# Performance work log

Measured on AMD Instinct MI355X. Metric: run time of the kernel, lower is better.

Reference implementation:

```python
import jax, jax.numpy as jnp
import numpy as np

B, T, C = 4, 2048, 768   # batch, seq, n_embd
E, K = 8, 2              # n_routed_experts, moe_top_k (expert hidden dim == C per source)


def setup_inputs() -> dict:
    key = jax.random.key(0)
    ks = jax.random.split(key, 6)
    s = 0.02  # init scale to keep relu(x)^2 well-behaved
    return {
        "x": jax.random.normal(ks[0], (B, T, C), jnp.float32),
        "w_fc_sh": jax.random.normal(ks[1], (C, C), jnp.float32) * s,    # shared expert c_fc (stored [in,out])
        "w_proj_sh": jax.random.normal(ks[2], (C, C), jnp.float32) * s,  # shared expert c_proj
        "w1": jax.random.normal(ks[3], (E, C, C), jnp.float32) * s,      # routed experts c_fc, [E,in,out]
        "w2": jax.random.normal(ks[4], (E, C, C), jnp.float32) * s,      # routed experts c_proj
        "router_w": jax.random.normal(ks[5], (E, C), jnp.float32) * s,   # router weight [E, C]
        "balance_bias": jnp.zeros((E,), jnp.float32),                    # router balance_bias buffer
    }


def _mlp(x, wfc, wproj):
    # MLP: c_proj(relu(c_fc(x))**2)
    h = jnp.square(jax.nn.relu(x @ wfc))
    return h @ wproj


def reference(x, w_fc_sh, w_proj_sh, w1, w2, router_w, balance_bias):
    Bx, Tx, Cx = x.shape
    shared = _mlp(x, w_fc_sh, w_proj_sh)                    # [B,T,C]

    xf = x.reshape(-1, Cx)                                  # [N,C]
    # --- router ---
    logits = xf.astype(jnp.float32) @ router_w.T            # [N,E]
    scores = jax.nn.sigmoid(logits)
    _, idx = jax.lax.top_k(scores + balance_bias, K)        # selection uses biased scores
    tw = jnp.take_along_axis(scores, idx, axis=-1)          # gate weights from unbiased scores
    tw = tw / (tw.sum(-1, keepdims=True) + 1e-20)           # [N,K]

    # per-token per-expert combine weights (equivalent to gather/MLP/index_add loop)
    combine = (jax.nn.one_hot(idx, E, dtype=tw.dtype) * tw[..., None]).sum(1)  # [N,E]

    # dense all-expert compute, masked combine (same math as sparse dispatch)
    h = jnp.square(jax.nn.relu(jnp.einsum('nc,ech->neh', xf, w1)))  # [N,E,H]
    y = jnp.einsum('neh,ehc->nec', h, w2)                            # [N,E,C]
    routed = jnp.einsum('nec,ne->nc', y, combine)                    # [N,C]

    return shared + routed.reshape(Bx, Tx, Cx)
```

## Files before the change

kernel.cpp:

```cpp
#include <hip/hip_runtime.h>
#include <stdint.h>

#define N_TOK 8192
#define C_DIM 768
#define E_NUM 8
#define NT2 (C_DIM / 64)
#define TOTX3 104
#define GRID3 312
#define XXP3 13

typedef short short8 __attribute__((ext_vector_type(8)));
typedef __bf16 bf16x8 __attribute__((ext_vector_type(8)));
typedef float f32x4 __attribute__((ext_vector_type(4)));

static __device__ __forceinline__ unsigned short f2bf(float f) {
    unsigned u = __float_as_uint(f);
    unsigned r = u + 0x7FFFu + ((u >> 16) & 1u);
    return (unsigned short)(r >> 16);
}
static __device__ __forceinline__ float bf2f(unsigned short h) {
    return __uint_as_float(((unsigned)h) << 16);
}

__global__ void wtrans_kernel(const float* __restrict__ wfc, const float* __restrict__ wpj,
                              const float* __restrict__ w1, const float* __restrict__ w2,
                              unsigned short* __restrict__ Wt) {
    __shared__ float tile[32][33];
    const int m = blockIdx.z;
    const float* src = (m == 0) ? wfc : (m == 1) ? wpj
                     : (m < 10) ? (w1 + (size_t)(m - 2) * C_DIM * C_DIM)
                                : (w2 + (size_t)(m - 10) * C_DIM * C_DIM);
    const int i0 = blockIdx.y * 32;
    const int o0 = blockIdx.x * 32;
    #pragma unroll
    for (int rr = 0; rr < 32; rr += 8)
        tile[threadIdx.y + rr][threadIdx.x] = src[(size_t)(i0 + threadIdx.y + rr) * C_DIM + o0 + threadIdx.x];
    __syncthreads();
    unsigned short* dst = Wt + (size_t)m * C_DIM * C_DIM;
    #pragma unroll
    for (int rr = 0; rr < 32; rr += 8) {
        int o = o0 + threadIdx.y + rr;
        dst[(size_t)o * C_DIM + i0 + threadIdx.x] = f2bf(tile[threadIdx.x][threadIdx.y + rr]);
    }
}

__global__ void router_kernel(const float* __restrict__ x, const float* __restrict__ rw,
                              const float* __restrict__ bias,
                              float* __restrict__ topk_w, int* __restrict__ eids,
                              unsigned short* __restrict__ xb) {
    const int wave = threadIdx.x >> 6;
    const int lane = threadIdx.x & 63;
    const int n = blockIdx.x * 4 + wave;
    const float* xp = x + (size_t)n * C_DIM + lane * 12;
    float xv[12];
    #pragma unroll
    for (int j = 0; j < 12; j++) xv[j] = xp[j];
    unsigned short* xbp = xb + (size_t)n * C_DIM + lane * 12;
    #pragma unroll
    for (int j = 0; j < 12; j++) xbp[j] = f2bf(xv[j]);
    float acc[E_NUM];
    #pragma unroll
    for (int e = 0; e < E_NUM; e++) acc[e] = 0.f;
    #pragma unroll
    for (int e = 0; e < E_NUM; e++) {
        const float* wp = rw + (size_t)e * C_DIM + lane * 12;
        #pragma unroll
        for (int j = 0; j < 12; j++) acc[e] += xv[j] * wp[j];
    }
    #pragma unroll
    for (int e = 0; e < E_NUM; e++) {
        #pragma unroll
        for (int off = 32; off > 0; off >>= 1) acc[e] += __shfl_xor(acc[e], off, 64);
    }
    if (lane == 0) {
        float sc[E_NUM];
        #pragma unroll
        for (int e = 0; e < E_NUM; e++) sc[e] = 1.f / (1.f + expf(-acc[e]));
        int e0 = 0; float best = -1e30f;
        #pragma unroll
        for (int e = 0; e < E_NUM; e++) { float v = sc[e] + bias[e]; if (v > best) { best = v; e0 = e; } }
        int e1 = -1; float best1 = -1e30f;
        #pragma unroll
        for (int e = 0; e < E_NUM; e++) { if (e == e0) continue; float v = sc[e] + bias[e]; if (v > best1) { best1 = v; e1 = e; } }
        float w0 = sc[e0], w1 = sc[e1];
        float s = w0 + w1 + 1e-20f;
        w0 /= s; w1 /= s;
        topk_w[n * 2] = w0; topk_w[n * 2 + 1] = w1;
        eids[n * 2] = e0; eids[n * 2 + 1] = e1;
    }
}

__global__ __launch_bounds__(1024) void bucketize_kernel(const int* __restrict__ eids,
                                                         int* __restrict__ counts,
                                                         int* __restrict__ buckets) {
    const int e = blockIdx.x;
    const int t = threadIdx.x;
    const int wv = t >> 6, lane = t & 63;
    __shared__ int wave_tot[16];
    int running = 0;
    for (int start = 0; start < 2 * N_TOK; start += 1024) {
        const int i = start + t;
        const int f = (eids[i] == e) ? 1 : 0;
        unsigned long long mask = __ballot(f);
        int pre = __popcll(mask & ((1ull << lane) - 1ull));
        if (lane == 0) wave_tot[wv] = __popcll(mask);
        __syncthreads();
        int wbase = 0, tot = 0;
        #pragma unroll
        for (int j = 0; j < 16; j++) { int c = wave_tot[j]; tot += c; if (j < wv) wbase += c; }
        if (f) buckets[e * N_TOK + running + wbase + pre] = i;
        running += tot;
        __syncthreads();
    }
    if (t == 0) counts[e] = running;
}

__global__ void prefix_kernel(const int* __restrict__ counts, int* __restrict__ xoffs) {
    if (threadIdx.x == 0 && blockIdx.x == 0) {
        int a = 0;
        for (int z = 0; z < E_NUM; z++) { xoffs[z] = a; a += (counts[z] + 255) >> 8; }
        xoffs[E_NUM] = a;
        xoffs[E_NUM + 1] = a + 32;
    }
}

#define GLOAD_LDS(g, l) __builtin_amdgcn_global_load_lds((const __attribute__((address_space(1))) void*)(g), (__attribute__((address_space(3))) void*)(l), 16, 0, 0)
#define WAITVM0() asm volatile("s_waitcnt vmcnt(0)" ::: "memory")
#define SCHEDB() __builtin_amdgcn_sched_barrier(0)
#define BAR() __builtin_amdgcn_s_barrier()

template <int PHASE>
__global__ __launch_bounds__(512, 2) void gemm_all_kernel(const unsigned short* __restrict__ Adir,
                                                          const unsigned short* __restrict__ Agat,
                                                          const unsigned short* __restrict__ WtAll,
                                                          void* __restrict__ dstDir,
                                                          unsigned short* __restrict__ dstGat,
                                                          const int* __restrict__ counts,
                                                          const int* __restrict__ buckets,
                                                          const int* __restrict__ xoffs) {
    const int fid = blockIdx.x;
    const int xcd = fid & 7;
    const int i3 = fid >> 3;
    const int xx = xcd * XXP3 + i3 / 3;
    const int y = i3 % 3;
    int xo[10];
    #pragma unroll
    for (int i = 0; i < 10; i++) xo[i] = xoffs[i];
    if (xx >= xo[9]) return;
    int z = E_NUM, xl = xx - xo[8];
    #pragma unroll
    for (int zz = 0; zz < E_NUM; zz++)
        if (xx >= xo[zz] && xx < xo[zz + 1]) { z = zz; xl = xx - xo[zz]; }
    const bool sh = (z == E_NUM);
    const int rows = sh ? N_TOK : counts[z];
    const int r0 = xl * 256;
    const int c0 = y * 256;

    __shared__ __align__(16) unsigned short lds[2 * 32768];

    const int t = threadIdx.x;
    const int lane = t & 63;
    const int wv = t >> 6;
    const int wm = wv >> 2;
    const int wn = wv & 3;

    const int widx = sh ? (PHASE == 0 ? 0 : 1) : (PHASE == 0 ? 2 + z : 10 + z);
    const unsigned short* Bmat = WtAll + (size_t)widx * C_DIM * C_DIM;
    const int* bk = buckets + z * N_TOK;

    const int srow = t >> 3;
    const int scol = (((t & 7) ^ ((t >> 3) & 7)) * 8);
    int grow[4];
    const unsigned short* Asrc;
    if (sh) {
        Asrc = Adir;
        #pragma unroll
        for (int c = 0; c < 4; c++) grow[c] = r0 + 64 * c + srow;
    } else {
        Asrc = Agat;
        #pragma unroll
        for (int c = 0; c < 4; c++) {
            int p = r0 + 64 * c + srow;
            int ev = bk[p < rows ? p : 0];
            grow[c] = (PHASE == 0) ? (ev >> 1) : ev;
        }
    }
    const unsigned short* ap[4];
    const unsigned short* bp[4];
    #pragma unroll
    for (int c = 0; c < 4; c++) {
        ap[c] = Asrc + (size_t)grow[c] * C_DIM + scol;
        bp[c] = Bmat + (size_t)(c0 + 64 * c + srow) * C_DIM + scol;
    }

    f32x4 acc[8][4];
    #pragma unroll
    for (int i = 0; i < 8; i++)
        #pragma unroll
        for (int j = 0; j < 4; j++) acc[i][j] = (f32x4){0.f, 0.f, 0.f, 0.f};

    const int fr = lane & 15;
    const int fq = lane >> 4;
    const int ks0 = ((fq ^ (fr & 7)) * 8);
    const int ks1 = (((4 + fq) ^ (fr & 7)) * 8);

    {
        unsigned short* d = lds + t * 8;
        #pragma unroll
        for (int c = 0; c < 4; c++) {
            GLOAD_LDS(ap[c], d + c * 4096);
            GLOAD_LDS(bp[c], d + 16384 + c * 4096);
        }
    }

    #pragma unroll
    for (int kt = 0; kt < NT2; ++kt) {
        WAITVM0();
        BAR();
        SCHEDB();
        if (kt + 1 < NT2) {
            unsigned short* d = lds + ((kt + 1) & 1) * 32768 + t * 8;
            const int ko = (kt + 1) * 64;
            #pragma unroll
            for (int c = 0; c < 4; c++) {
                GLOAD_LDS(ap[c] + ko, d + c * 4096);
                GLOAD_LDS(bp[c] + ko, d + 16384 + c * 4096);
            }
        }
        SCHEDB();
        const unsigned short* buf = lds + (kt & 1) * 32768;
        short8 bfr[4][2];
        #pragma unroll
        for (int j = 0; j < 4; j++) {
            const unsigned short* rp = buf + 16384 + (size_t)(wn * 64 + j * 16 + fr) * 64;
            bfr[j][0] = *reinterpret_cast<const short8*>(rp + ks0);
            bfr[j][1] = *reinterpret_cast<const short8*>(rp + ks1);
        }
        __builtin_amdgcn_s_setprio(1);
        #pragma unroll
        for (int i = 0; i < 8; i++) {
            const unsigned short* rp = buf + (size_t)(wm * 128 + i * 16 + fr) * 64;
            short8 a0 = *reinterpret_cast<const short8*>(rp + ks0);
            short8 a1 = *reinterpret_cast<const short8*>(rp + ks1);
            #pragma unroll
            for (int j = 0; j < 4; j++)
                acc[i][j] = __builtin_amdgcn_mfma_f32_16x16x32_bf16(
                    __builtin_bit_cast(bf16x8, a0), __builtin_bit_cast(bf16x8, bfr[j][0]), acc[i][j], 0, 0, 0);
            #pragma unroll
            for (int j = 0; j < 4; j++)
                acc[i][j] = __builtin_amdgcn_mfma_f32_16x16x32_bf16(
                    __builtin_bit_cast(bf16x8, a1), __builtin_bit_cast(bf16x8, bfr[j][1]), acc[i][j], 0, 0, 0);
        }
        __builtin_amdgcn_s_setprio(0);
    }

    const int orow = r0 + wm * 128;
    const int ocol = c0 + wn * 64;
    if (sh) {
        if constexpr (PHASE == 0) {
            unsigned short* Hd = (unsigned short*)dstDir;
            #pragma unroll
            for (int i = 0; i < 8; i++)
                #pragma unroll
                for (int rr = 0; rr < 4; rr++) {
                    size_t base = (size_t)(orow + i * 16 + fq * 4 + rr) * C_DIM;
                    #pragma unroll
                    for (int j = 0; j < 4; j++) {
                        float v = acc[i][j][rr];
                        float rl = v > 0.f ? v : 0.f;
                        Hd[base + ocol + j * 16 + fr] = f2bf(rl * rl);
                    }
                }
        } else {
            float* od = (float*)dstDir;
            #pragma unroll
            for (int i = 0; i < 8; i++)
                #pragma unroll
                for (int rr = 0; rr < 4; rr++) {
                    size_t base = (size_t)(orow + i * 16 + fq * 4 + rr) * C_DIM;
                    #pragma unroll
                    for (int j = 0; j < 4; j++)
                        od[base + ocol + j * 16 + fr] = acc[i][j][rr];
                }
        }
    } else {
        #pragma unroll
        for (int i = 0; i < 8; i++)
            #pragma unroll
            for (int rr = 0; rr < 4; rr++) {
                int pos = orow + i * 16 + fq * 4 + rr;
                if (pos < rows) {
                    int ent = bk[pos];
                    size_t base = (size_t)ent * C_DIM;
                    #pragma unroll
                    for (int j = 0; j < 4; j++) {
                        float v = acc[i][j][rr];
                        if (PHASE == 0) {
                            float rl = v > 0.f ? v : 0.f;
                            dstGat[base + ocol + j * 16 + fr] = f2bf(rl * rl);
                        } else {
                            dstGat[base + ocol + j * 16 + fr] = f2bf(v);
                        }
                    }
                }
            }
    }
}

__global__ void combine_kernel(float* __restrict__ out, const unsigned short* __restrict__ Y,
                               const float* __restrict__ tw) {
    int idx = blockIdx.x * blockDim.x + threadIdx.x;
    const int per_row = C_DIM / 4;
    if (idx >= N_TOK * per_row) return;
    int n = idx / per_row;
    int c = (idx % per_row) * 4;
    float w0 = tw[n * 2], w1 = tw[n * 2 + 1];
    const ushort4 a = *reinterpret_cast<const ushort4*>(Y + (size_t)(n * 2) * C_DIM + c);
    const ushort4 b = *reinterpret_cast<const ushort4*>(Y + (size_t)(n * 2 + 1) * C_DIM + c);
    float4* op = reinterpret_cast<float4*>(out + (size_t)n * C_DIM + c);
    float4 o = *op;
    o.x += w0 * bf2f(a.x) + w1 * bf2f(b.x);
    o.y += w0 * bf2f(a.y) + w1 * bf2f(b.y);
    o.z += w0 * bf2f(a.z) + w1 * bf2f(b.z);
    o.w += w0 * bf2f(a.w) + w1 * bf2f(b.w);
    *op = o;
}

extern "C" void kernel_launch(void* const* d_in, const int* in_sizes, int n_in,
                              void* d_out, int out_size, void* d_ws, size_t ws_size,
                              hipStream_t stream) {
    const float* x   = (const float*)d_in[0];
    const float* wfc = (const float*)d_in[1];
    const float* wpj = (const float*)d_in[2];
    const float* w1  = (const float*)d_in[3];
    const float* w2  = (const float*)d_in[4];
    const float* rw  = (const float*)d_in[5];
    const float* bias= (const float*)d_in[6];
    float* out = (float*)d_out;

    char* ws = (char*)d_ws;
    size_t off = 0;
    auto alloc = [&](size_t bytes) { void* p = ws + off; off += (bytes + 255) & ~(size_t)255; return p; };
    unsigned short* xb   = (unsigned short*)alloc((size_t)N_TOK * C_DIM * 2);
    unsigned short* Wt   = (unsigned short*)alloc((size_t)18 * C_DIM * C_DIM * 2);
    unsigned short* H    = (unsigned short*)alloc((size_t)N_TOK * 2 * C_DIM * 2);
    unsigned short* Hsh  = (unsigned short*)alloc((size_t)N_TOK * C_DIM * 2);
    unsigned short* Y    = (unsigned short*)alloc((size_t)N_TOK * 2 * C_DIM * 2);
    float* topk_w        = (float*)alloc((size_t)N_TOK * 2 * 4);
    int* counts          = (int*)alloc(256);
    int* buckets         = (int*)alloc((size_t)E_NUM * N_TOK * 4);
    int* eids            = (int*)alloc((size_t)2 * N_TOK * 4);
    int* xoffs           = (int*)alloc(64);

    wtrans_kernel<<<dim3(24, 24, 18), dim3(32, 8), 0, stream>>>(wfc, wpj, w1, w2, Wt);
    router_kernel<<<N_TOK / 4, 256, 0, stream>>>(x, rw, bias, topk_w, eids, xb);
    bucketize_kernel<<<E_NUM, 1024, 0, stream>>>(eids, counts, buckets);
    prefix_kernel<<<1, 64, 0, stream>>>(counts, xoffs);

    gemm_all_kernel<0><<<GRID3, 512, 0, stream>>>(xb, xb, Wt, Hsh, H, counts, buckets, xoffs);
    gemm_all_kernel<1><<<GRID3, 512, 0, stream>>>(Hsh, H, Wt, out, Y, counts, buckets, xoffs);

    combine_kernel<<<(N_TOK * (C_DIM / 4) + 255) / 256, 256, 0, stream>>>(out, Y, topk_w);
}
```

Measured before the change: 156.8 us.

## Switch GEMM mainloop to 4-stage K=32 pipeline with partial vmcnt waits

Restructures the GEMM main loop from a double-buffered K=64 tile to a four-buffer ring of K=32 tiles, prefetching three stages ahead. Waits use partial vmcnt counts so later loads stay in flight. The LDS swizzle and staging layout change to fit the 32-wide rows. The goal is to hide global-load latency better. The cost is twice as many barriers and loop iterations with half the MFMA work between them, and a different LDS bank-conflict pattern.

```diff
diff --git a/kernel.cpp b/kernel.cpp
--- a/kernel.cpp
+++ b/kernel.cpp
@@ -4,7 +4,7 @@
 #define N_TOK 8192
 #define C_DIM 768
 #define E_NUM 8
-#define NT2 (C_DIM / 64)
+#define NT32 24
 #define TOTX3 104
 #define GRID3 312
 #define XXP3 13
@@ -125,7 +125,7 @@
 }
 
 #define GLOAD_LDS(g, l) __builtin_amdgcn_global_load_lds((const __attribute__((address_space(1))) void*)(g), (__attribute__((address_space(3))) void*)(l), 16, 0, 0)
-#define WAITVM0() asm volatile("s_waitcnt vmcnt(0)" ::: "memory")
+#define WAITVM(n) asm volatile("s_waitcnt vmcnt(" #n ")" ::: "memory")
 #define SCHEDB() __builtin_amdgcn_sched_barrier(0)
 #define BAR() __builtin_amdgcn_s_barrier()
 
@@ -156,7 +156,7 @@
     const int r0 = xl * 256;
     const int c0 = y * 256;
 
-    __shared__ __align__(16) unsigned short lds[2 * 32768];
+    __shared__ __align__(16) unsigned short lds[4 * 16384];
 
     const int t = threadIdx.x;
     const int lane = t & 63;
@@ -168,30 +168,25 @@
     const unsigned short* Bmat = WtAll + (size_t)widx * C_DIM * C_DIM;
     const int* bk = buckets + z * N_TOK;
 
-    const int srow = t >> 3;
-    const int scol = (((t & 7) ^ ((t >> 3) & 7)) * 8);
-    int grow[4];
+    const int srow = t >> 2;
+    const int scol = (((t & 3) ^ ((t >> 3) & 3)) * 8);
+    int grow0, grow1;
     const unsigned short* Asrc;
     if (sh) {
         Asrc = Adir;
-        #pragma unroll
-        for (int c = 0; c < 4; c++) grow[c] = r0 + 64 * c + srow;
+        grow0 = r0 + srow; grow1 = r0 + 128 + srow;
     } else {
         Asrc = Agat;
-        #pragma unroll
-        for (int c = 0; c < 4; c++) {
-            int p = r0 + 64 * c + srow;
-            int ev = bk[p < rows ? p : 0];
-            grow[c] = (PHASE == 0) ? (ev >> 1) : ev;
-        }
-    }
-    const unsigned short* ap[4];
-    const unsigned short* bp[4];
-    #pragma unroll
-    for (int c = 0; c < 4; c++) {
-        ap[c] = Asrc + (size_t)grow[c] * C_DIM + scol;
-        bp[c] = Bmat + (size_t)(c0 + 64 * c + srow) * C_DIM + scol;
-    }
+        int p0 = r0 + srow, p1 = r0 + 128 + srow;
+        int e0v = bk[p0 < rows ? p0 : 0];
+        int e1v = bk[p1 < rows ? p1 : 0];
+        grow0 = (PHASE == 0) ? (e0v >> 1) : e0v;
+        grow1 = (PHASE == 0) ? (e1v >> 1) : e1v;
+    }
+    const unsigned short* ap0 = Asrc + (size_t)grow0 * C_DIM + scol;
+    const unsigned short* ap1 = Asrc + (size_t)grow1 * C_DIM + scol;
+    const unsigned short* bp0 = Bmat + (size_t)(c0 + srow) * C_DIM + scol;
+    const unsigned short* bp1 = Bmat + (size_t)(c0 + 128 + srow) * C_DIM + scol;
 
     f32x4 acc[8][4];
     #pragma unroll
@@ -201,55 +196,47 @@
 
     const int fr = lane & 15;
     const int fq = lane >> 4;
-    const int ks0 = ((fq ^ (fr & 7)) * 8);
-    const int ks1 = (((4 + fq) ^ (fr & 7)) * 8);
-
-    {
-        unsigned short* d = lds + t * 8;
-        #pragma unroll
-        for (int c = 0; c < 4; c++) {
-            GLOAD_LDS(ap[c], d + c * 4096);
-            GLOAD_LDS(bp[c], d + 16384 + c * 4096);
-        }
-    }
-
-    #pragma unroll
-    for (int kt = 0; kt < NT2; ++kt) {
-        WAITVM0();
+    const int ks = ((fq ^ ((fr >> 1) & 3)) * 8);
+
+    #pragma unroll
+    for (int p = 0; p < 3; ++p) {
+        unsigned short* d = lds + p * 16384 + t * 8;
+        const int ko = p * 32;
+        GLOAD_LDS(ap0 + ko, d);
+        GLOAD_LDS(ap1 + ko, d + 4096);
+        GLOAD_LDS(bp0 + ko, d + 8192);
+        GLOAD_LDS(bp1 + ko, d + 12288);
+    }
+
+    #pragma unroll
+    for (int kt = 0; kt < NT32; ++kt) {
+        if (kt + 2 < NT32)      { WAITVM(8); }
+        else if (kt + 1 < NT32) { WAITVM(4); }
+        else                    { WAITVM(0); }
         BAR();
         SCHEDB();
-        if (kt + 1 < NT2) {
-            unsigned short* d = lds + ((kt + 1) & 1) * 32768 + t * 8;
-            const int ko = (kt + 1) * 64;
-            #pragma unroll
-            for (int c = 0; c < 4; c++) {
-                GLOAD_LDS(ap[c] + ko, d + c * 4096);
-                GLOAD_LDS(bp[c] + ko, d + 16384 + c * 4096);
-            }
+        if (kt + 3 < NT32) {
+            unsigned short* d = lds + ((kt + 3) & 3) * 16384 + t * 8;
+            const int ko = (kt + 3) * 32;
+            GLOAD_LDS(ap0 + ko, d);
+            GLOAD_LDS(ap1 + ko, d + 4096);
+            GLOAD_LDS(bp0 + ko, d + 8192);
+            GLOAD_LDS(bp1 + ko, d + 12288);
         }
         SCHEDB();
-        const unsigned short* buf = lds + (kt & 1) * 32768;
-        short8 bfr[4][2];
-        #pragma unroll
-        for (int j = 0; j < 4; j++) {
-            const unsigned short* rp = buf + 16384 + (size_t)(wn * 64 + j * 16 + fr) * 64;
-            bfr[j][0] = *reinterpret_cast<const short8*>(rp + ks0);
-            bfr[j][1] = *reinterpret_cast<const short8*>(rp + ks1);
-        }
+        const unsigned short* buf = lds + (kt & 3) * 16384;
+        short8 bfr[4];
+        #pragma unroll
+        for (int j = 0; j < 4; j++)
+            bfr[j] = *reinterpret_cast<const short8*>(buf + 8192 + (size_t)(wn * 64 + j * 16 + fr) * 32 + ks);
         __builtin_amdgcn_s_setprio(1);
         #pragma unroll
         for (int i = 0; i < 8; i++) {
-            const unsigned short* rp = buf + (size_t)(wm * 128 + i * 16 + fr) * 64;
-            short8 a0 = *reinterpret_cast<const short8*>(rp + ks0);
-            short8 a1 = *reinterpret_cast<const short8*>(rp + ks1);
+            short8 a = *reinterpret_cast<const short8*>(buf + (size_t)(wm * 128 + i * 16 + fr) * 32 + ks);
             #pragma unroll
             for (int j = 0; j < 4; j++)
                 acc[i][j] = __builtin_amdgcn_mfma_f32_16x16x32_bf16(
-                    __builtin_bit_cast(bf16x8, a0), __builtin_bit_cast(bf16x8, bfr[j][0]), acc[i][j], 0, 0, 0);
-            #pragma unroll
-            for (int j = 0; j < 4; j++)
-                acc[i][j] = __builtin_amdgcn_mfma_f32_16x16x32_bf16(
-                    __builtin_bit_cast(bf16x8, a1), __builtin_bit_cast(bf16x8, bfr[j][1]), acc[i][j], 0, 0, 0);
+                    __builtin_bit_cast(bf16x8, a), __builtin_bit_cast(bf16x8, bfr[j]), acc[i][j], 0, 0, 0);
         }
         __builtin_amdgcn_s_setprio(0);
     }
```

Result: no change. 158.5 us (+1.1%).
